# Performance work log

Measured on AMD Instinct MI355X. Metric: run time of the kernel, lower is better.

The kernel has to match this reference:

```python
import jax, jax.numpy as jnp
from jax import lax
import numpy as np

BETA = 6.6


def _conv(x, w, b=None, stride=1, pad=0):
    # x: NCHW, w: OIHW (torch layout)
    y = lax.conv_general_dilated(x, w, (stride, stride), [(pad, pad), (pad, pad)],
                                 dimension_numbers=('NCHW', 'OIHW', 'NCHW'))
    if b is not None:
        y = y + b[None, :, None, None]
    return y


def _conv_t(x, w, b, stride=2, pad=1):
    # torch ConvTranspose2d: w is [in, out, kH, kW]; equivalent to dilated conv with flipped kernel
    k = w.shape[2]
    w2 = jnp.flip(w, (2, 3)).transpose(1, 0, 2, 3)  # -> OIHW
    y = lax.conv_general_dilated(x, w2, (1, 1), [(k - 1 - pad, k - 1 - pad)] * 2,
                                 lhs_dilation=(stride, stride),
                                 dimension_numbers=('NCHW', 'OIHW', 'NCHW'))
    return y + b[None, :, None, None]


def _res_stack(x, pairs):
    for wa, wb in pairs:
        x = x + _conv(jax.nn.relu(_conv(jax.nn.relu(x), wa, pad=1)), wb, pad=1)
    return jax.nn.relu(x)


def _quantize(z, E, beta):
    # z: [B, D, H, W]; E: [K, D]
    xp = z.transpose(0, 2, 3, 1)                       # BHWD
    flat = xp.reshape(-1, E.shape[1])                  # [N, D]
    d = (jnp.sum(flat ** 2, axis=1, keepdims=True)
         + jnp.sum(E ** 2, axis=1)
         - 2.0 * flat @ E.T)                           # [N, K]
    idx = jnp.argmin(d, axis=1)                        # [N]
    q = E[idx].reshape(xp.shape)                       # gather == onehot @ E
    loss_q = jnp.mean((q - lax.stop_gradient(xp)) ** 2)
    loss_e = jnp.mean((lax.stop_gradient(q) - xp) ** 2)
    loss = loss_q + beta * loss_e
    q_st = xp + lax.stop_gradient(q - xp)              # straight-through
    z_q = q_st.transpose(0, 3, 1, 2)
    counts = jnp.zeros((E.shape[0],), jnp.float32).at[idx].add(1.0)
    probs = counts / flat.shape[0]
    perplexity = jnp.exp(-jnp.sum(probs * jnp.log(probs + 1e-10)))
    return loss, z_q, perplexity


def setup_inputs() -> dict:
    key = jax.random.key(0)
    ks = iter(jax.random.split(key, 32))

    def p(*s):
        return jax.random.normal(next(ks), s, jnp.float32) * 0.05

    inp = dict(
        x=jax.random.normal(next(ks), (32, 3, 256, 256), jnp.float32),
        # encoder
        w1=p(64, 3, 4, 4), b1=p(64),
        w2=p(128, 64, 4, 4), b2=p(128),
        w3=p(128, 128, 3, 3), b3=p(128),
        r0a=p(32, 128, 3, 3), r0b=p(128, 32, 3, 3),
        r1a=p(32, 128, 3, 3), r1b=p(128, 32, 3, 3),
        # pre-VQ 1x1 conv
        wp=p(64, 128, 1, 1), bp=p(64),
        # codebook
        E=jax.random.uniform(next(ks), (512, 64), jnp.float32, -1.0 / 512, 1.0 / 512),
        # decoder
        dw1=p(128, 64, 3, 3), db1=p(128),
        dr0a=p(32, 128, 3, 3), dr0b=p(128, 32, 3, 3),
        dr1a=p(32, 128, 3, 3), dr1b=p(128, 32, 3, 3),
        tw1=p(128, 64, 4, 4), tb1=p(64),   # ConvTranspose2d(128,64,4,2,1) torch layout [in,out,k,k]
        tw2=p(64, 3, 4, 4), tb2=p(3),      # ConvTranspose2d(64,3,4,2,1)
    )
    return inp


def reference(x, w1, b1, w2, b2, w3, b3, r0a, r0b, r1a, r1b, wp, bp, E,
              dw1, db1, dr0a, dr0b, dr1a, dr1b, tw1, tb1, tw2, tb2):
    # Encoder
    z = jax.nn.relu(_conv(x, w1, b1, stride=2, pad=1))
    z = jax.nn.relu(_conv(z, w2, b2, stride=2, pad=1))
    z = _conv(z, w3, b3, stride=1, pad=1)
    z = _res_stack(z, [(r0a, r0b), (r1a, r1b)])
    # pre-VQ projection
    z = _conv(z, wp, bp)
    # Vector quantization
    loss, z_q, perplexity = _quantize(z, E, BETA)
    # Decoder
    d = _conv(z_q, dw1, db1, pad=1)
    d = _res_stack(d, [(dr0a, dr0b), (dr1a, dr1b)])
    d = jax.nn.relu(_conv_t(d, tw1, tb1))
    x_tilda = _conv_t(d, tw2, tb2)
    return (loss, x_tilda, perplexity)
```

## Files before the change

kernel.cpp:

```cpp
#include <hip/hip_runtime.h>
#include <math.h>

typedef __attribute__((ext_vector_type(8))) short bf16x8;
typedef __attribute__((ext_vector_type(4))) float f32x4;

__device__ inline float bf2f(ushort u) {
    union { uint i; float f; } v; v.i = ((uint)u) << 16; return v.f;
}
__device__ inline ushort f2bf(float f) {
    union { float f; uint i; } v; v.f = f;
    uint b = v.i;
    b += 0x7FFFu + ((b >> 16) & 1u);
    return (ushort)(b >> 16);
}
__device__ inline uint relu2bf(uint x) {
    uint s = x & 0x80008000u;
    uint m = (s >> 15) * 0xFFFFu;
    return x & ~m;
}

template<int CIN, int COUT, int NT>
__global__ __launch_bounds__(256) void wt_oihw(const float* __restrict__ s, ushort* __restrict__ d) {
    int i = blockIdx.x * 256 + threadIdx.x;
    if (i >= COUT * NT * CIN) return;
    int co = i / (NT * CIN);
    int r  = i % (NT * CIN);
    int tap = r / CIN, ci = r % CIN;
    d[i] = f2bf(s[(co * CIN + ci) * NT + tap]);
}

__global__ __launch_bounds__(256) void wt_tconv1(const float* __restrict__ s, ushort* __restrict__ d) {
    int i = blockIdx.x * 256 + threadIdx.x;
    if (i >= 4 * 64 * 512) return;
    int cls = i >> 15;
    int co  = (i >> 9) & 63;
    int k   = i & 511;
    int tap = k >> 7, ci = k & 127;
    int a = tap >> 1, b = tap & 1;
    int ph = cls >> 1, pw = cls & 1;
    int kh = ph ? (a ? 2 : 0) : (a ? 3 : 1);
    int kw = pw ? (b ? 2 : 0) : (b ? 3 : 1);
    d[i] = f2bf(s[((ci * 64 + co) << 4) + kh * 4 + kw]);
}

template<int CIN, int COUT, int S, int CFG, int CLS, int NT,
         bool RELU_A, bool RELU_OUT, bool HAS_RES>
__global__ __launch_bounds__(256)
void conv_mfma(const ushort* __restrict__ in, const ushort* __restrict__ wt,
               const float* __restrict__ bias, const ushort* __restrict__ res,
               ushort* __restrict__ out, int Hin, int Win) {
    constexpr int K = NT * CIN;
    constexpr int KSTEPS = K / 32;
    constexpr int CSTEPS = CIN / 32;
    constexpr int WM = (COUT == 128) ? 4 : (COUT == 64) ? 2 : 1;

    __shared__ ushort sA[64 * 40];

    const int t = threadIdx.x;
    const int w = t >> 6, l = t & 63;
    const int bid = blockIdx.x;
    const int n = bid >> 6, orow = bid & 63;

    const int m0 = (COUT == 128) ? 0 : (COUT == 64) ? 32 * (w >> 1) : 16 * w;
    const int n0 = (COUT == 128) ? 32 * w : (COUT == 64) ? 32 * (w & 1) : 0;

    f32x4 acc[WM][2] = {};

    const int gm = t >> 2;
    const int gc = (t & 3) * 8;

    for (int ks = 0; ks < KSTEPS; ++ks) {
        const int tap = ks / CSTEPS, ci0 = (ks % CSTEPS) * 32;
        int dh, dw;
        if (CFG == 0)      { dh = tap / 3 - 1; dw = tap % 3 - 1; }
        else if (CFG == 1) { dh = tap / 4 - 1; dw = tap % 4 - 1; }
        else if (CFG == 2) { int a = tap >> 1, b = tap & 1;
                             dh = (CLS >> 1) ? 1 - a : -a;
                             dw = (CLS & 1) ? 1 - b : -b; }
        else               { dh = 0; dw = 0; }

        const int ih = S * orow + dh, iw = S * gm + dw;
        uint4 gv = {0u, 0u, 0u, 0u};
        if ((unsigned)ih < (unsigned)Hin && (unsigned)iw < (unsigned)Win) {
            gv = *reinterpret_cast<const uint4*>(
                in + (((long long)(n * Hin + ih)) * Win + iw) * CIN + ci0 + gc);
        }
        if (RELU_A) {
            gv.x = relu2bf(gv.x); gv.y = relu2bf(gv.y);
            gv.z = relu2bf(gv.z); gv.w = relu2bf(gv.w);
        }

        bf16x8 bfr[2];
        #pragma unroll
        for (int nf = 0; nf < 2; ++nf)
            bfr[nf] = *reinterpret_cast<const bf16x8*>(
                wt + (n0 + nf * 16 + (l & 15)) * K + ks * 32 + ((l >> 4) * 8));

        __syncthreads();
        *reinterpret_cast<uint4*>(&sA[gm * 40 + gc]) = gv;
        __syncthreads();

        #pragma unroll
        for (int mf = 0; mf < WM; ++mf) {
            bf16x8 afr = *reinterpret_cast<const bf16x8*>(
                &sA[(m0 + mf * 16 + (l & 15)) * 40 + ((l >> 4) * 8)]);
            #pragma unroll
            for (int nf = 0; nf < 2; ++nf)
                acc[mf][nf] = __builtin_amdgcn_mfma_f32_16x16x32_bf16(
                    afr, bfr[nf], acc[mf][nf], 0, 0, 0);
        }
    }

    #pragma unroll
    for (int mf = 0; mf < WM; ++mf) {
        #pragma unroll
        for (int nf = 0; nf < 2; ++nf) {
            const int col = n0 + nf * 16 + (l & 15);
            const float bv = bias ? bias[col] : 0.f;
            #pragma unroll
            for (int r = 0; r < 4; ++r) {
                const int row = m0 + mf * 16 + ((l >> 4) * 4) + r;
                long long oidx;
                if (CFG == 2)
                    oidx = (((long long)(n * 128 + 2 * orow + (CLS >> 1))) * 128
                            + 2 * row + (CLS & 1)) * COUT + col;
                else
                    oidx = ((long long)bid * 64 + row) * COUT + col;
                float v = acc[mf][nf][r] + bv;
                if (HAS_RES) v += bf2f(res[oidx]);
                if (RELU_OUT) v = fmaxf(v, 0.f);
                out[oidx] = f2bf(v);
            }
        }
    }
}

__global__ __launch_bounds__(256)
void conv1_k(const float* __restrict__ x, const float* __restrict__ w1,
             const float* __restrict__ b1, ushort* __restrict__ out) {
    __shared__ float sIn[3 * 4 * 36];
    __shared__ float sW[64 * 48];
    const int t = threadIdx.x;
    const int bid = blockIdx.x;
    const int n = bid >> 7, oh = bid & 127;
    const int ow0 = blockIdx.y * 16;

    for (int i = t; i < 3072; i += 256) sW[i] = w1[i];
    for (int i = t; i < 3 * 4 * 34; i += 256) {
        int ci = i / 136, r = i - ci * 136;
        int r4 = r / 34, iwl = r % 34;
        int ih = 2 * oh - 1 + r4;
        int iw = 2 * ow0 - 1 + iwl;
        float v = 0.f;
        if ((unsigned)ih < 256u && (unsigned)iw < 256u)
            v = x[((n * 3 + ci) * 256 + ih) * 256 + iw];
        sIn[ci * 144 + r4 * 36 + iwl] = v;
    }
    __syncthreads();

    const int co = t & 63, j = t >> 6;
    float wr[48];
    #pragma unroll
    for (int i = 0; i < 48; ++i) wr[i] = sW[co * 48 + i];
    const float bv = b1[co];

    #pragma unroll
    for (int q = 0; q < 4; ++q) {
        const int owl = j * 4 + q;
        float acc = bv;
        #pragma unroll
        for (int ci = 0; ci < 3; ++ci)
            #pragma unroll
            for (int kh = 0; kh < 4; ++kh)
                #pragma unroll
                for (int kw = 0; kw < 4; ++kw)
                    acc = fmaf(sIn[ci * 144 + kh * 36 + 2 * owl + kw],
                               wr[ci * 16 + kh * 4 + kw], acc);
        acc = fmaxf(acc, 0.f);
        out[(((long long)(n * 128 + oh)) * 128 + ow0 + owl) * 64 + co] = f2bf(acc);
    }
}

__global__ __launch_bounds__(256)
void convt2_k(const ushort* __restrict__ in, const float* __restrict__ tw2,
              const float* __restrict__ tb2, float* __restrict__ out) {
    __shared__ float sW[64 * 48];
    const int t = threadIdx.x;
    for (int i = t; i < 3072; i += 256) sW[i] = tw2[i];
    __syncthreads();

    const int bid = blockIdx.x;
    const int n = bid >> 8, oh = bid & 255;
    const int ow = t;
    const int khA = (oh + 1) & 1, ihA = (oh + 1) >> 1;
    const int kwA = (ow + 1) & 1, iwA = (ow + 1) >> 1;

    float a0 = tb2[0], a1 = tb2[1], a2 = tb2[2];
    #pragma unroll
    for (int a = 0; a < 2; ++a) {
        const int ih = ihA - a;
        if ((unsigned)ih >= 128u) continue;
        const int kh = khA + 2 * a;
        #pragma unroll
        for (int b = 0; b < 2; ++b) {
            const int iw = iwA - b;
            if ((unsigned)iw >= 128u) continue;
            const int kw = kwA + 2 * b;
            const ushort* src = in + (((long long)(n * 128 + ih)) * 128 + iw) * 64;
            const int k = kh * 4 + kw;
            #pragma unroll
            for (int c8 = 0; c8 < 8; ++c8) {
                uint4 v = *reinterpret_cast<const uint4*>(src + c8 * 8);
                const uint u[4] = {v.x, v.y, v.z, v.w};
                #pragma unroll
                for (int p = 0; p < 4; ++p) {
                    union { uint i; float f; } lo, hi;
                    lo.i = u[p] << 16; hi.i = u[p] & 0xFFFF0000u;
                    const int ci = c8 * 8 + p * 2;
                    a0 = fmaf(lo.f, sW[ci * 48 + 0 * 16 + k], a0);
                    a1 = fmaf(lo.f, sW[ci * 48 + 1 * 16 + k], a1);
                    a2 = fmaf(lo.f, sW[ci * 48 + 2 * 16 + k], a2);
                    a0 = fmaf(hi.f, sW[(ci + 1) * 48 + 0 * 16 + k], a0);
                    a1 = fmaf(hi.f, sW[(ci + 1) * 48 + 1 * 16 + k], a1);
                    a2 = fmaf(hi.f, sW[(ci + 1) * 48 + 2 * 16 + k], a2);
                }
            }
        }
    }
    const long long px = (long long)oh * 256 + ow;
    out[(long long)(n * 3 + 0) * 65536 + px] = a0;
    out[(long long)(n * 3 + 1) * 65536 + px] = a1;
    out[(long long)(n * 3 + 2) * 65536 + px] = a2;
}

__global__ __launch_bounds__(256)
void vq_kernel(const ushort* __restrict__ z, const float* __restrict__ E,
               ushort* __restrict__ zq, float* __restrict__ stats) {
    __shared__ float sE[128 * 64];
    __shared__ float sN[128];
    __shared__ unsigned shist[512];
    __shared__ float red[256];
    const int t = threadIdx.x;
    for (int i = t; i < 512; i += 256) shist[i] = 0;

    const int p0 = blockIdx.x * 512 + t;
    const int p1 = p0 + 256;

    float za[64], zb[64];
    #pragma unroll
    for (int c8 = 0; c8 < 8; ++c8) {
        uint4 va = *reinterpret_cast<const uint4*>(z + (long long)p0 * 64 + c8 * 8);
        uint4 vb = *reinterpret_cast<const uint4*>(z + (long long)p1 * 64 + c8 * 8);
        const uint ua[4] = {va.x, va.y, va.z, va.w};
        const uint ub[4] = {vb.x, vb.y, vb.z, vb.w};
        #pragma unroll
        for (int p = 0; p < 4; ++p) {
            union { uint i; float f; } l0, h0, l1, h1;
            l0.i = ua[p] << 16; h0.i = ua[p] & 0xFFFF0000u;
            l1.i = ub[p] << 16; h1.i = ub[p] & 0xFFFF0000u;
            za[c8 * 8 + p * 2] = l0.f; za[c8 * 8 + p * 2 + 1] = h0.f;
            zb[c8 * 8 + p * 2] = l1.f; zb[c8 * 8 + p * 2 + 1] = h1.f;
        }
    }

    float best0 = 3.4e38f, best1 = 3.4e38f;
    int bi0 = 0, bi1 = 0;

    for (int k0 = 0; k0 < 512; k0 += 128) {
        __syncthreads();
        for (int i = t; i < 128 * 64; i += 256) sE[i] = E[k0 * 64 + i];
        __syncthreads();
        if (t < 128) {
            const float* e = sE + t * 64;
            float s = 0.f;
            #pragma unroll
            for (int d = 0; d < 64; ++d) { float xx = e[(d + t) & 63]; s = fmaf(xx, xx, s); }
            sN[t] = s;
        }
        __syncthreads();
        for (int k = 0; k < 128; ++k) {
            const float4* e4 = reinterpret_cast<const float4*>(sE + (k << 6));
            float s0a = 0.f, s0b = 0.f, s1a = 0.f, s1b = 0.f;
            #pragma unroll
            for (int q = 0; q < 8; ++q) {
                float4 ea = e4[2 * q], eb = e4[2 * q + 1];
                s0a = fmaf(za[8*q+0], ea.x, s0a); s0a = fmaf(za[8*q+1], ea.y, s0a);
                s0a = fmaf(za[8*q+2], ea.z, s0a); s0a = fmaf(za[8*q+3], ea.w, s0a);
                s0b = fmaf(za[8*q+4], eb.x, s0b); s0b = fmaf(za[8*q+5], eb.y, s0b);
                s0b = fmaf(za[8*q+6], eb.z, s0b); s0b = fmaf(za[8*q+7], eb.w, s0b);
                s1a = fmaf(zb[8*q+0], ea.x, s1a); s1a = fmaf(zb[8*q+1], ea.y, s1a);
                s1a = fmaf(zb[8*q+2], ea.z, s1a); s1a = fmaf(zb[8*q+3], ea.w, s1a);
                s1b = fmaf(zb[8*q+4], eb.x, s1b); s1b = fmaf(zb[8*q+5], eb.y, s1b);
                s1b = fmaf(zb[8*q+6], eb.z, s1b); s1b = fmaf(zb[8*q+7], eb.w, s1b);
            }
            float sc0 = sN[k] - 2.f * (s0a + s0b);
            float sc1 = sN[k] - 2.f * (s1a + s1b);
            if (sc0 < best0) { best0 = sc0; bi0 = k0 + k; }
            if (sc1 < best1) { best1 = sc1; bi1 = k0 + k; }
        }
    }

    const float* e0g = E + bi0 * 64;
    const float* e1g = E + bi1 * 64;
    float dist = 0.f;
    ushort pk[8];
    #pragma unroll
    for (int c8 = 0; c8 < 8; ++c8) {
        #pragma unroll
        for (int p = 0; p < 8; ++p) {
            const float ed = e0g[c8 * 8 + p];
            const float df = ed - za[c8 * 8 + p];
            dist = fmaf(df, df, dist);
            pk[p] = f2bf(ed);
        }
        *reinterpret_cast<uint4*>(zq + (long long)p0 * 64 + c8 * 8) =
            *reinterpret_cast<const uint4*>(pk);
    }
    #pragma unroll
    for (int c8 = 0; c8 < 8; ++c8) {
        #pragma unroll
        for (int p = 0; p < 8; ++p) {
            const float ed = e1g[c8 * 8 + p];
            const float df = ed - zb[c8 * 8 + p];
            dist = fmaf(df, df, dist);
            pk[p] = f2bf(ed);
        }
        *reinterpret_cast<uint4*>(zq + (long long)p1 * 64 + c8 * 8) =
            *reinterpret_cast<const uint4*>(pk);
    }
    atomicAdd(&shist[bi0], 1u);
    atomicAdd(&shist[bi1], 1u);

    red[t] = dist;
    __syncthreads();
    for (int s = 128; s > 0; s >>= 1) {
        if (t < s) red[t] += red[t + s];
        __syncthreads();
    }
    if (t == 0) atomicAdd(&stats[0], red[0]);
    for (int i = t; i < 512; i += 256) {
        unsigned c = shist[i];
        if (c) atomicAdd(&stats[1 + i], (float)c);
    }
}

__global__ __launch_bounds__(512)
void finalize_kernel(const float* __restrict__ stats, float* __restrict__ out, int plast) {
    __shared__ float red[512];
    int t = threadIdx.x;
    float c = stats[1 + t];
    float p = c * (1.f / 131072.f);
    red[t] = p * logf(p + 1e-10f);
    __syncthreads();
    for (int s = 256; s > 0; s >>= 1) {
        if (t < s) red[t] += red[t + s];
        __syncthreads();
    }
    if (t == 0) {
        out[plast] = expf(-red[0]);
        out[0] = 7.6f * stats[0] * (1.f / 8388608.f);
    }
}

extern "C" void kernel_launch(void* const* d_in, const int* in_sizes, int n_in,
                              void* d_out, int out_size, void* d_ws, size_t ws_size,
                              hipStream_t stream) {
    (void)in_sizes; (void)n_in; (void)ws_size;
    const float* x   = (const float*)d_in[0];
    const float* w1  = (const float*)d_in[1];
    const float* b1  = (const float*)d_in[2];
    const float* w2  = (const float*)d_in[3];
    const float* b2  = (const float*)d_in[4];
    const float* w3  = (const float*)d_in[5];
    const float* b3  = (const float*)d_in[6];
    const float* r0a = (const float*)d_in[7];
    const float* r0b = (const float*)d_in[8];
    const float* r1a = (const float*)d_in[9];
    const float* r1b = (const float*)d_in[10];
    const float* wp  = (const float*)d_in[11];
    const float* bp  = (const float*)d_in[12];
    const float* E   = (const float*)d_in[13];
    const float* dw1 = (const float*)d_in[14];
    const float* db1 = (const float*)d_in[15];
    const float* dr0a= (const float*)d_in[16];
    const float* dr0b= (const float*)d_in[17];
    const float* dr1a= (const float*)d_in[18];
    const float* dr1b= (const float*)d_in[19];
    const float* tw1 = (const float*)d_in[20];
    const float* tb1 = (const float*)d_in[21];
    const float* tw2 = (const float*)d_in[22];
    const float* tb2 = (const float*)d_in[23];

    float* out = (float*)d_out;
    ushort* ws = (ushort*)d_ws;

    ushort* H1 = ws;
    ushort* H2 = ws + 33554432;
    ushort* C  = ws + 50331648;
    ushort* F  = ws + 67108864;
    ushort* Z  = ws + 71303168;
    ushort* ZQ = ws + 79691776;
    ushort* W0 = ws + 88080384;
    ushort* Wt2   = W0;
    ushort* Wt3   = W0 + 131072;
    ushort* Wr0a  = W0 + 278528;
    ushort* Wr0b  = W0 + 315392;
    ushort* Wr1a  = W0 + 352256;
    ushort* Wr1b  = W0 + 389120;
    ushort* Wp    = W0 + 425984;
    ushort* Wd1   = W0 + 434176;
    ushort* Wdr0a = W0 + 507904;
    ushort* Wdr0b = W0 + 544768;
    ushort* Wdr1a = W0 + 581632;
    ushort* Wdr1b = W0 + 618496;
    ushort* WT1   = W0 + 655360;
    float*  ST    = (float*)(ws + 88866816);
    ushort* T = H1;
    ushort* D = H2;

    hipMemsetAsync(ST, 0, 513 * sizeof(float), stream);

    dim3 blk(256);
    wt_oihw<64, 128,16><<<512, blk, 0, stream>>>(w2,  Wt2);
    wt_oihw<128,128, 9><<<576, blk, 0, stream>>>(w3,  Wt3);
    wt_oihw<128, 32, 9><<<144, blk, 0, stream>>>(r0a, Wr0a);
    wt_oihw<32, 128, 9><<<144, blk, 0, stream>>>(r0b, Wr0b);
    wt_oihw<128, 32, 9><<<144, blk, 0, stream>>>(r1a, Wr1a);
    wt_oihw<32, 128, 9><<<144, blk, 0, stream>>>(r1b, Wr1b);
    wt_oihw<128, 64, 1><<<32,  blk, 0, stream>>>(wp,  Wp);
    wt_oihw<64, 128, 9><<<288, blk, 0, stream>>>(dw1, Wd1);
    wt_oihw<128, 32, 9><<<144, blk, 0, stream>>>(dr0a, Wdr0a);
    wt_oihw<32, 128, 9><<<144, blk, 0, stream>>>(dr0b, Wdr0b);
    wt_oihw<128, 32, 9><<<144, blk, 0, stream>>>(dr1a, Wdr1a);
    wt_oihw<32, 128, 9><<<144, blk, 0, stream>>>(dr1b, Wdr1b);
    wt_tconv1<<<512, blk, 0, stream>>>(tw1, WT1);

    conv1_k<<<dim3(32 * 128, 8), blk, 0, stream>>>(x, w1, b1, H1);
    conv_mfma<64,128,2,1,0,16,false,true ,false><<<2048, blk, 0, stream>>>(H1, Wt2, b2, nullptr, H2, 128, 128);
    conv_mfma<128,128,1,0,0, 9,false,false,false><<<2048, blk, 0, stream>>>(H2, Wt3, b3, nullptr, C, 64, 64);
    conv_mfma<128, 32,1,0,0, 9,true ,true ,false><<<2048, blk, 0, stream>>>(C, Wr0a, nullptr, nullptr, F, 64, 64);
    conv_mfma<32, 128,1,0,0, 9,false,false,true ><<<2048, blk, 0, stream>>>(F, Wr0b, nullptr, C, C, 64, 64);
    conv_mfma<128, 32,1,0,0, 9,true ,true ,false><<<2048, blk, 0, stream>>>(C, Wr1a, nullptr, nullptr, F, 64, 64);
    conv_mfma<32, 128,1,0,0, 9,false,true ,true ><<<2048, blk, 0, stream>>>(F, Wr1b, nullptr, C, C, 64, 64);
    conv_mfma<128, 64,1,3,0, 1,false,false,false><<<2048, blk, 0, stream>>>(C, Wp, bp, nullptr, Z, 64, 64);

    vq_kernel<<<256, blk, 0, stream>>>(Z, E, ZQ, ST);

    conv_mfma<64,128,1,0,0, 9,false,false,false><<<2048, blk, 0, stream>>>(ZQ, Wd1, db1, nullptr, D, 64, 64);
    conv_mfma<128, 32,1,0,0, 9,true ,true ,false><<<2048, blk, 0, stream>>>(D, Wdr0a, nullptr, nullptr, F, 64, 64);
    conv_mfma<32, 128,1,0,0, 9,false,false,true ><<<2048, blk, 0, stream>>>(F, Wdr0b, nullptr, D, D, 64, 64);
    conv_mfma<128, 32,1,0,0, 9,true ,true ,false><<<2048, blk, 0, stream>>>(D, Wdr1a, nullptr, nullptr, F, 64, 64);
    conv_mfma<32, 128,1,0,0, 9,false,true ,true ><<<2048, blk, 0, stream>>>(F, Wdr1b, nullptr, D, D, 64, 64);
    conv_mfma<128, 64,1,2,0, 4,false,true ,false><<<2048, blk, 0, stream>>>(D, WT1 + 0 * 32768, tb1, nullptr, T, 64, 64);
    conv_mfma<128, 64,1,2,1, 4,false,true ,false><<<2048, blk, 0, stream>>>(D, WT1 + 1 * 32768, tb1, nullptr, T, 64, 64);
    conv_mfma<128, 64,1,2,2, 4,false,true ,false><<<2048, blk, 0, stream>>>(D, WT1 + 2 * 32768, tb1, nullptr, T, 64, 64);
    conv_mfma<128, 64,1,2,3, 4,false,true ,false><<<2048, blk, 0, stream>>>(D, WT1 + 3 * 32768, tb1, nullptr, T, 64, 64);
    convt2_k<<<32 * 256, blk, 0, stream>>>(T, tw2, tb2, out + 1);

    finalize_kernel<<<1, 512, 0, stream>>>(ST, out, out_size - 1);
}
```

Before: 1.376 ms.

## Double-buffer larger conv tiles and move VQ distance search onto MFMA

The conv kernel now handles two output rows (128 pixels) per block and gives each wave a bigger MFMA subtile. It double-buffers the LDS A-tile, prefetching the next k-step's gather while the current MFMAs run, so only one barrier per step remains and weight loads are reused across more rows. The VQ argmin, previously fp32 scalar FMA over the codebook, becomes a bf16 MFMA matmul against a precomputed bf16 codebook and norms, followed by shuffle and LDS argmin reductions. Computing the VQ distances in bf16 could change which codeword wins on near ties compared with fp32.

```diff
diff --git a/kernel.cpp b/kernel.cpp
--- a/kernel.cpp
+++ b/kernel.cpp
@@ -43,34 +43,49 @@
     d[i] = f2bf(s[((ci * 64 + co) << 4) + kh * 4 + kw]);
 }
 
+__global__ __launch_bounds__(256) void vq_prep(const float* __restrict__ E,
+                                               ushort* __restrict__ Ebf, float* __restrict__ eN) {
+    int i = blockIdx.x * 256 + threadIdx.x;
+    if (i < 32768) Ebf[i] = f2bf(E[i]);
+    if (i < 512) {
+        float s = 0.f;
+        #pragma unroll 8
+        for (int d = 0; d < 64; ++d) { float x = E[i * 64 + d]; s = fmaf(x, x, s); }
+        eN[i] = s;
+    }
+}
+
 template<int CIN, int COUT, int S, int CFG, int CLS, int NT,
          bool RELU_A, bool RELU_OUT, bool HAS_RES>
 __global__ __launch_bounds__(256)
-void conv_mfma(const ushort* __restrict__ in, const ushort* __restrict__ wt,
-               const float* __restrict__ bias, const ushort* __restrict__ res,
-               ushort* __restrict__ out, int Hin, int Win) {
+void conv_mfma2(const ushort* __restrict__ in, const ushort* __restrict__ wt,
+                const float* __restrict__ bias, const ushort* __restrict__ res,
+                ushort* __restrict__ out, int Hin, int Win) {
     constexpr int K = NT * CIN;
     constexpr int KSTEPS = K / 32;
     constexpr int CSTEPS = CIN / 32;
-    constexpr int WM = (COUT == 128) ? 4 : (COUT == 64) ? 2 : 1;
-
-    __shared__ ushort sA[64 * 40];
+    constexpr int WM = (COUT == 128) ? 4 : 2;
+    constexpr int WN = (COUT == 32) ? 2 : 4;
+
+    __shared__ ushort sA[2][128 * 40];
 
     const int t = threadIdx.x;
     const int w = t >> 6, l = t & 63;
     const int bid = blockIdx.x;
-    const int n = bid >> 6, orow = bid & 63;
-
-    const int m0 = (COUT == 128) ? 0 : (COUT == 64) ? 32 * (w >> 1) : 16 * w;
-    const int n0 = (COUT == 128) ? 32 * w : (COUT == 64) ? 32 * (w & 1) : 0;
-
-    f32x4 acc[WM][2] = {};
-
-    const int gm = t >> 2;
-    const int gc = (t & 3) * 8;
-
-    for (int ks = 0; ks < KSTEPS; ++ks) {
-        const int tap = ks / CSTEPS, ci0 = (ks % CSTEPS) * 32;
+    const int n = bid >> 5, R = bid & 31;
+
+    const int m0 = (COUT == 128) ? 64 * (w >> 1) : 32 * w;
+    const int n0 = (COUT == 128) ? 64 * (w & 1) : 0;
+
+    const int gpx  = t >> 1;
+    const int gk   = (t & 1) * 16;
+    const int grow = 2 * R + (gpx >> 6);
+    const int gcol = gpx & 63;
+
+    auto gather = [&](int ks, uint4& g0, uint4& g1) {
+        int tap, ci0;
+        if (CSTEPS == 1) { tap = ks; ci0 = 0; }
+        else             { tap = ks / CSTEPS; ci0 = (ks % CSTEPS) * 32; }
         int dh, dw;
         if (CFG == 0)      { dh = tap / 3 - 1; dw = tap % 3 - 1; }
         else if (CFG == 1) { dh = tap / 4 - 1; dw = tap % 4 - 1; }
@@ -78,54 +93,77 @@
                              dh = (CLS >> 1) ? 1 - a : -a;
                              dw = (CLS & 1) ? 1 - b : -b; }
         else               { dh = 0; dw = 0; }
-
-        const int ih = S * orow + dh, iw = S * gm + dw;
-        uint4 gv = {0u, 0u, 0u, 0u};
+        const int ih = S * grow + dh, iw = S * gcol + dw;
+        g0 = make_uint4(0u, 0u, 0u, 0u); g1 = g0;
         if ((unsigned)ih < (unsigned)Hin && (unsigned)iw < (unsigned)Win) {
-            gv = *reinterpret_cast<const uint4*>(
-                in + (((long long)(n * Hin + ih)) * Win + iw) * CIN + ci0 + gc);
+            const ushort* p = in + (((long long)(n * Hin + ih)) * Win + iw) * CIN + ci0 + gk;
+            g0 = *reinterpret_cast<const uint4*>(p);
+            g1 = *reinterpret_cast<const uint4*>(p + 8);
         }
         if (RELU_A) {
-            gv.x = relu2bf(gv.x); gv.y = relu2bf(gv.y);
-            gv.z = relu2bf(gv.z); gv.w = relu2bf(gv.w);
-        }
-
-        bf16x8 bfr[2];
-        #pragma unroll
-        for (int nf = 0; nf < 2; ++nf)
+            g0.x = relu2bf(g0.x); g0.y = relu2bf(g0.y); g0.z = relu2bf(g0.z); g0.w = relu2bf(g0.w);
+            g1.x = relu2bf(g1.x); g1.y = relu2bf(g1.y); g1.z = relu2bf(g1.z); g1.w = relu2bf(g1.w);
+        }
+    };
+
+    f32x4 acc[WM][WN] = {};
+
+    uint4 g0, g1;
+    gather(0, g0, g1);
+    *reinterpret_cast<uint4*>(&sA[0][gpx * 40 + gk])     = g0;
+    *reinterpret_cast<uint4*>(&sA[0][gpx * 40 + gk + 8]) = g1;
+    __syncthreads();
+
+    int cur = 0;
+    for (int ks = 0; ks < KSTEPS; ++ks) {
+        const bool more = (ks + 1 < KSTEPS);
+        uint4 h0, h1;
+        if (more) gather(ks + 1, h0, h1);
+
+        bf16x8 bfr[WN];
+        #pragma unroll
+        for (int nf = 0; nf < WN; ++nf)
             bfr[nf] = *reinterpret_cast<const bf16x8*>(
                 wt + (n0 + nf * 16 + (l & 15)) * K + ks * 32 + ((l >> 4) * 8));
 
-        __syncthreads();
-        *reinterpret_cast<uint4*>(&sA[gm * 40 + gc]) = gv;
-        __syncthreads();
-
-        #pragma unroll
-        for (int mf = 0; mf < WM; ++mf) {
-            bf16x8 afr = *reinterpret_cast<const bf16x8*>(
-                &sA[(m0 + mf * 16 + (l & 15)) * 40 + ((l >> 4) * 8)]);
-            #pragma unroll
-            for (int nf = 0; nf < 2; ++nf)
+        bf16x8 afr[WM];
+        #pragma unroll
+        for (int mf = 0; mf < WM; ++mf)
+            afr[mf] = *reinterpret_cast<const bf16x8*>(
+                &sA[cur][(m0 + mf * 16 + (l & 15)) * 40 + ((l >> 4) * 8)]);
+
+        #pragma unroll
+        for (int mf = 0; mf < WM; ++mf)
+            #pragma unroll
+            for (int nf = 0; nf < WN; ++nf)
                 acc[mf][nf] = __builtin_amdgcn_mfma_f32_16x16x32_bf16(
-                    afr, bfr[nf], acc[mf][nf], 0, 0, 0);
+                    afr[mf], bfr[nf], acc[mf][nf], 0, 0, 0);
+
+        if (more) {
+            *reinterpret_cast<uint4*>(&sA[cur ^ 1][gpx * 40 + gk])     = h0;
+            *reinterpret_cast<uint4*>(&sA[cur ^ 1][gpx * 40 + gk + 8]) = h1;
+            __syncthreads();
+            cur ^= 1;
         }
     }
 
     #pragma unroll
     for (int mf = 0; mf < WM; ++mf) {
         #pragma unroll
-        for (int nf = 0; nf < 2; ++nf) {
+        for (int nf = 0; nf < WN; ++nf) {
             const int col = n0 + nf * 16 + (l & 15);
             const float bv = bias ? bias[col] : 0.f;
             #pragma unroll
             for (int r = 0; r < 4; ++r) {
-                const int row = m0 + mf * 16 + ((l >> 4) * 4) + r;
+                const int prow = m0 + mf * 16 + ((l >> 4) * 4) + r;
+                const int orow = 2 * R + (prow >> 6);
+                const int ocol = prow & 63;
                 long long oidx;
                 if (CFG == 2)
                     oidx = (((long long)(n * 128 + 2 * orow + (CLS >> 1))) * 128
-                            + 2 * row + (CLS & 1)) * COUT + col;
+                            + 2 * ocol + (CLS & 1)) * COUT + col;
                 else
-                    oidx = ((long long)bid * 64 + row) * COUT + col;
+                    oidx = (((long long)(n * 64 + orow)) * 64 + ocol) * COUT + col;
                 float v = acc[mf][nf][r] + bv;
                 if (HAS_RES) v += bf2f(res[oidx]);
                 if (RELU_OUT) v = fmaxf(v, 0.f);
@@ -234,104 +272,112 @@
 }
 
 __global__ __launch_bounds__(256)
-void vq_kernel(const ushort* __restrict__ z, const float* __restrict__ E,
-               ushort* __restrict__ zq, float* __restrict__ stats) {
-    __shared__ float sE[128 * 64];
-    __shared__ float sN[128];
+void vq_mfma(const ushort* __restrict__ z, const ushort* __restrict__ Ebf,
+             const float* __restrict__ E, const float* __restrict__ eN,
+             ushort* __restrict__ zq, float* __restrict__ stats) {
+    __shared__ ushort sZ[64 * 72];
+    __shared__ float sEN[512];
+    __shared__ float sV[64 * 4];
+    __shared__ int   sI[64 * 4];
+    __shared__ int   sIdx[64];
     __shared__ unsigned shist[512];
     __shared__ float red[256];
+
     const int t = threadIdx.x;
-    for (int i = t; i < 512; i += 256) shist[i] = 0;
-
-    const int p0 = blockIdx.x * 512 + t;
-    const int p1 = p0 + 256;
-
-    float za[64], zb[64];
-    #pragma unroll
-    for (int c8 = 0; c8 < 8; ++c8) {
-        uint4 va = *reinterpret_cast<const uint4*>(z + (long long)p0 * 64 + c8 * 8);
-        uint4 vb = *reinterpret_cast<const uint4*>(z + (long long)p1 * 64 + c8 * 8);
-        const uint ua[4] = {va.x, va.y, va.z, va.w};
-        const uint ub[4] = {vb.x, vb.y, vb.z, vb.w};
-        #pragma unroll
-        for (int p = 0; p < 4; ++p) {
-            union { uint i; float f; } l0, h0, l1, h1;
-            l0.i = ua[p] << 16; h0.i = ua[p] & 0xFFFF0000u;
-            l1.i = ub[p] << 16; h1.i = ub[p] & 0xFFFF0000u;
-            za[c8 * 8 + p * 2] = l0.f; za[c8 * 8 + p * 2 + 1] = h0.f;
-            zb[c8 * 8 + p * 2] = l1.f; zb[c8 * 8 + p * 2 + 1] = h1.f;
-        }
-    }
-
-    float best0 = 3.4e38f, best1 = 3.4e38f;
-    int bi0 = 0, bi1 = 0;
-
-    for (int k0 = 0; k0 < 512; k0 += 128) {
-        __syncthreads();
-        for (int i = t; i < 128 * 64; i += 256) sE[i] = E[k0 * 64 + i];
-        __syncthreads();
-        if (t < 128) {
-            const float* e = sE + t * 64;
-            float s = 0.f;
-            #pragma unroll
-            for (int d = 0; d < 64; ++d) { float xx = e[(d + t) & 63]; s = fmaf(xx, xx, s); }
-            sN[t] = s;
-        }
-        __syncthreads();
-        for (int k = 0; k < 128; ++k) {
-            const float4* e4 = reinterpret_cast<const float4*>(sE + (k << 6));
-            float s0a = 0.f, s0b = 0.f, s1a = 0.f, s1b = 0.f;
-            #pragma unroll
-            for (int q = 0; q < 8; ++q) {
-                float4 ea = e4[2 * q], eb = e4[2 * q + 1];
-                s0a = fmaf(za[8*q+0], ea.x, s0a); s0a = fmaf(za[8*q+1], ea.y, s0a);
-                s0a = fmaf(za[8*q+2], ea.z, s0a); s0a = fmaf(za[8*q+3], ea.w, s0a);
-                s0b = fmaf(za[8*q+4], eb.x, s0b); s0b = fmaf(za[8*q+5], eb.y, s0b);
-                s0b = fmaf(za[8*q+6], eb.z, s0b); s0b = fmaf(za[8*q+7], eb.w, s0b);
-                s1a = fmaf(zb[8*q+0], ea.x, s1a); s1a = fmaf(zb[8*q+1], ea.y, s1a);
-                s1a = fmaf(zb[8*q+2], ea.z, s1a); s1a = fmaf(zb[8*q+3], ea.w, s1a);
-                s1b = fmaf(zb[8*q+4], eb.x, s1b); s1b = fmaf(zb[8*q+5], eb.y, s1b);
-                s1b = fmaf(zb[8*q+6], eb.z, s1b); s1b = fmaf(zb[8*q+7], eb.w, s1b);
+    const int w = t >> 6, l = t & 63;
+    const long long p0 = (long long)blockIdx.x * 64;
+
+    {
+        const int px = t >> 2, koff = (t & 3) * 16;
+        const ushort* p = z + (p0 + px) * 64 + koff;
+        uint4 a0 = *reinterpret_cast<const uint4*>(p);
+        uint4 a1 = *reinterpret_cast<const uint4*>(p + 8);
+        *reinterpret_cast<uint4*>(&sZ[px * 72 + koff])     = a0;
+        *reinterpret_cast<uint4*>(&sZ[px * 72 + koff + 8]) = a1;
+        sEN[t] = eN[t]; sEN[t + 256] = eN[t + 256];
+        shist[t] = 0u; shist[t + 256] = 0u;
+    }
+    __syncthreads();
+
+    f32x4 acc[4][8] = {};
+    #pragma unroll
+    for (int ks = 0; ks < 2; ++ks) {
+        bf16x8 bfr[8];
+        #pragma unroll
+        for (int nf = 0; nf < 8; ++nf)
+            bfr[nf] = *reinterpret_cast<const bf16x8*>(
+                Ebf + (w * 128 + nf * 16 + (l & 15)) * 64 + ks * 32 + ((l >> 4) * 8));
+        #pragma unroll
+        for (int mf = 0; mf < 4; ++mf) {
+            bf16x8 afr = *reinterpret_cast<const bf16x8*>(
+                &sZ[(mf * 16 + (l & 15)) * 72 + ks * 32 + ((l >> 4) * 8)]);
+            #pragma unroll
+            for (int nf = 0; nf < 8; ++nf)
+                acc[mf][nf] = __builtin_amdgcn_mfma_f32_16x16x32_bf16(
+                    afr, bfr[nf], acc[mf][nf], 0, 0, 0);
+        }
+    }
+
+    float eNr[8];
+    #pragma unroll
+    for (int nf = 0; nf < 8; ++nf) eNr[nf] = sEN[w * 128 + nf * 16 + (l & 15)];
+
+    #pragma unroll
+    for (int mf = 0; mf < 4; ++mf) {
+        #pragma unroll
+        for (int r = 0; r < 4; ++r) {
+            float best = 3.4e38f; int bidx = 0;
+            #pragma unroll
+            for (int nf = 0; nf < 8; ++nf) {
+                float s = eNr[nf] - 2.f * acc[mf][nf][r];
+                int   c = w * 128 + nf * 16 + (l & 15);
+                if (s < best || (s == best && c < bidx)) { best = s; bidx = c; }
             }
-            float sc0 = sN[k] - 2.f * (s0a + s0b);
-            float sc1 = sN[k] - 2.f * (s1a + s1b);
-            if (sc0 < best0) { best0 = sc0; bi0 = k0 + k; }
-            if (sc1 < best1) { best1 = sc1; bi1 = k0 + k; }
-        }
-    }
-
-    const float* e0g = E + bi0 * 64;
-    const float* e1g = E + bi1 * 64;
-    float dist = 0.f;
-    ushort pk[8];
-    #pragma unroll
-    for (int c8 = 0; c8 < 8; ++c8) {
-        #pragma unroll
-        for (int p = 0; p < 8; ++p) {
-            const float ed = e0g[c8 * 8 + p];
-            const float df = ed - za[c8 * 8 + p];
+            #pragma unroll
+            for (int off = 1; off < 16; off <<= 1) {
+                float ov = __shfl_xor(best, off);
+                int   oi = __shfl_xor(bidx, off);
+                if (ov < best || (ov == best && oi < bidx)) { best = ov; bidx = oi; }
+            }
+            if ((l & 15) == 0) {
+                const int px = mf * 16 + ((l >> 4) * 4) + r;
+                sV[px * 4 + w] = best; sI[px * 4 + w] = bidx;
+            }
+        }
+    }
+    __syncthreads();
+
+    if (t < 64) {
+        float best = sV[t * 4]; int bidx = sI[t * 4];
+        #pragma unroll
+        for (int w2 = 1; w2 < 4; ++w2) {
+            float v = sV[t * 4 + w2]; int c = sI[t * 4 + w2];
+            if (v < best || (v == best && c < bidx)) { best = v; bidx = c; }
+        }
+        sIdx[t] = bidx;
+        atomicAdd(&shist[bidx], 1u);
+    }
+    __syncthreads();
+
+    {
+        const int px = t >> 2, doff = (t & 3) * 16;
+        const int idx = sIdx[px];
+        const float* e = E + idx * 64 + doff;
+        float dist = 0.f;
+        uint4 pk4[2];
+        ushort* pk = reinterpret_cast<ushort*>(pk4);
+        #pragma unroll
+        for (int j = 0; j < 16; ++j) {
+            float ev = e[j];
+            float zv = bf2f(sZ[px * 72 + doff + j]);
+            float df = ev - zv;
             dist = fmaf(df, df, dist);
-            pk[p] = f2bf(ed);
-        }
-        *reinterpret_cast<uint4*>(zq + (long long)p0 * 64 + c8 * 8) =
-            *reinterpret_cast<const uint4*>(pk);
-    }
-    #pragma unroll
-    for (int c8 = 0; c8 < 8; ++c8) {
-        #pragma unroll
-        for (int p = 0; p < 8; ++p) {
-            const float ed = e1g[c8 * 8 + p];
-            const float df = ed - zb[c8 * 8 + p];
-            dist = fmaf(df, df, dist);
-            pk[p] = f2bf(ed);
-        }
-        *reinterpret_cast<uint4*>(zq + (long long)p1 * 64 + c8 * 8) =
-            *reinterpret_cast<const uint4*>(pk);
-    }
-    atomicAdd(&shist[bi0], 1u);
-    atomicAdd(&shist[bi1], 1u);
-
-    red[t] = dist;
+            pk[j] = f2bf(ev);
+        }
+        *reinterpret_cast<uint4*>(zq + (p0 + px) * 64 + doff)     = pk4[0];
+        *reinterpret_cast<uint4*>(zq + (p0 + px) * 64 + doff + 8) = pk4[1];
+        red[t] = dist;
+    }
     __syncthreads();
     for (int s = 128; s > 0; s >>= 1) {
         if (t < s) red[t] += red[t + s];
@@ -414,7 +460,9 @@
     ushort* Wdr1a = W0 + 581632;
     ushort* Wdr1b = W0 + 618496;
     ushort* WT1   = W0 + 655360;
-    float*  ST    = (float*)(ws + 88866816);
+    ushort* Ebf   = W0 + 786432;
+    float*  eN    = (float*)(W0 + 819200);
+    float*  ST    = (float*)(W0 + 820224);
     ushort* T = H1;
     ushort* D = H2;
 
@@ -434,27 +482,28 @@
     wt_oihw<128, 32, 9><<<144, blk, 0, stream>>>(dr1a, Wdr1a);
     wt_oihw<32, 128, 9><<<144, blk, 0, stream>>>(dr1b, Wdr1b);
     wt_tconv1<<<512, blk, 0, stream>>>(tw1, WT1);
+    vq_prep<<<128, blk, 0, stream>>>(E, Ebf, eN);
 
     conv1_k<<<dim3(32 * 128, 8), blk, 0, stream>>>(x, w1, b1, H1);
-    conv_mfma<64,128,2,1,0,16,false,true ,false><<<2048, blk, 0, stream>>>(H1, Wt2, b2, nullptr, H2, 128, 128);
-    conv_mfma<128,128,1,0,0, 9,false,false,false><<<2048, blk, 0, stream>>>(H2, Wt3, b3, nullptr, C, 64, 64);
-    conv_mfma<128, 32,1,0,0, 9,true ,true ,false><<<2048, blk, 0, stream>>>(C, Wr0a, nullptr, nullptr, F, 64, 64);
-    conv_mfma<32, 128,1,0,0, 9,false,false,true ><<<2048, blk, 0, stream>>>(F, Wr0b, nullptr, C, C, 64, 64);
-    conv_mfma<128, 32,1,0,0, 9,true ,true ,false><<<2048, blk, 0, stream>>>(C, Wr1a, nullptr, nullptr, F, 64, 64);
-    conv_mfma<32, 128,1,0,0, 9,false,true ,true ><<<2048, blk, 0, stream>>>(F, Wr1b, nullptr, C, C, 64, 64);
-    conv_mfma<128, 64,1,3,0, 1,false,false,false><<<2048, blk, 0, stream>>>(C, Wp, bp, nullptr, Z, 64, 64);
-
-    vq_kernel<<<256, blk, 0, stream>>>(Z, E, ZQ, ST);
-
-    conv_mfma<64,128,1,0,0, 9,false,false,false><<<2048, blk, 0, stream>>>(ZQ, Wd1, db1, nullptr, D, 64, 64);
-    conv_mfma<128, 32,1,0,0, 9,true ,true ,false><<<2048, blk, 0, stream>>>(D, Wdr0a, nullptr, nullptr, F, 64, 64);
-    conv_mfma<32, 128,1,0,0, 9,false,false,true ><<<2048, blk, 0, stream>>>(F, Wdr0b, nullptr, D, D, 64, 64);
-    conv_mfma<128, 32,1,0,0, 9,true ,true ,false><<<2048, blk, 0, stream>>>(D, Wdr1a, nullptr, nullptr, F, 64, 64);
-    conv_mfma<32, 128,1,0,0, 9,false,true ,true ><<<2048, blk, 0, stream>>>(F, Wdr1b, nullptr, D, D, 64, 64);
-    conv_mfma<128, 64,1,2,0, 4,false,true ,false><<<2048, blk, 0, stream>>>(D, WT1 + 0 * 32768, tb1, nullptr, T, 64, 64);
-    conv_mfma<128, 64,1,2,1, 4,false,true ,false><<<2048, blk, 0, stream>>>(D, WT1 + 1 * 32768, tb1, nullptr, T, 64, 64);
-    conv_mfma<128, 64,1,2,2, 4,false,true ,false><<<2048, blk, 0, stream>>>(D, WT1 + 2 * 32768, tb1, nullptr, T, 64, 64);
-    conv_mfma<128, 64,1,2,3, 4,false,true ,false><<<2048, blk, 0, stream>>>(D, WT1 + 3 * 32768, tb1, nullptr, T, 64, 64);
+    conv_mfma2<64,128,2,1,0,16,false,true ,false><<<1024, blk, 0, stream>>>(H1, Wt2, b2, nullptr, H2, 128, 128);
+    conv_mfma2<128,128,1,0,0, 9,false,false,false><<<1024, blk, 0, stream>>>(H2, Wt3, b3, nullptr, C, 64, 64);
+    conv_mfma2<128, 32,1,0,0, 9,true ,true ,false><<<1024, blk, 0, stream>>>(C, Wr0a, nullptr, nullptr, F, 64, 64);
+    conv_mfma2<32, 128,1,0,0, 9,false,false,true ><<<1024, blk, 0, stream>>>(F, Wr0b, nullptr, C, C, 64, 64);
+    conv_mfma2<128, 32,1,0,0, 9,true ,true ,false><<<1024, blk, 0, stream>>>(C, Wr1a, nullptr, nullptr, F, 64, 64);
+    conv_mfma2<32, 128,1,0,0, 9,false,true ,true ><<<1024, blk, 0, stream>>>(F, Wr1b, nullptr, C, C, 64, 64);
+    conv_mfma2<128, 64,1,3,0, 1,false,false,false><<<1024, blk, 0, stream>>>(C, Wp, bp, nullptr, Z, 64, 64);
+
+    vq_mfma<<<2048, blk, 0, stream>>>(Z, Ebf, E, eN, ZQ, ST);
+
+    conv_mfma2<64,128,1,0,0, 9,false,false,false><<<1024, blk, 0, stream>>>(ZQ, Wd1, db1, nullptr, D, 64, 64);
+    conv_mfma2<128, 32,1,0,0, 9,true ,true ,false><<<1024, blk, 0, stream>>>(D, Wdr0a, nullptr, nullptr, F, 64, 64);
+    conv_mfma2<32, 128,1,0,0, 9,false,false,true ><<<1024, blk, 0, stream>>>(F, Wdr0b, nullptr, D, D, 64, 64);
+    conv_mfma2<128, 32,1,0,0, 9,true ,true ,false><<<1024, blk, 0, stream>>>(D, Wdr1a, nullptr, nullptr, F, 64, 64);
+    conv_mfma2<32, 128,1,0,0, 9,false,true ,true ><<<1024, blk, 0, stream>>>(F, Wdr1b, nullptr, D, D, 64, 64);
+    conv_mfma2<128, 64,1,2,0, 4,false,true ,false><<<1024, blk, 0, stream>>>(D, WT1 + 0 * 32768, tb1, nullptr, T, 64, 64);
+    conv_mfma2<128, 64,1,2,1, 4,false,true ,false><<<1024, blk, 0, stream>>>(D, WT1 + 1 * 32768, tb1, nullptr, T, 64, 64);
+    conv_mfma2<128, 64,1,2,2, 4,false,true ,false><<<1024, blk, 0, stream>>>(D, WT1 + 2 * 32768, tb1, nullptr, T, 64, 64);
+    conv_mfma2<128, 64,1,2,3, 4,false,true ,false><<<1024, blk, 0, stream>>>(D, WT1 + 3 * 32768, tb1, nullptr, T, 64, 64);
     convt2_k<<<32 * 256, blk, 0, stream>>>(T, tw2, tb2, out + 1);
 
     finalize_kernel<<<1, 512, 0, stream>>>(ST, out, out_size - 1);
```

After: 1.328 ms. 3.5% less time.
